# Performance work log

Measured on AMD Instinct MI355X. Metric: run time of the kernel, lower is better.

## Reference

```python
import jax, jax.numpy as jnp
import numpy as np

B, S, D, E, K = 4, 2048, 1024, 8, 2
DF = 4 * D


def setup_inputs() -> dict:
    key = jax.random.key(0)
    ks = jax.random.split(key, 7)
    x = jax.random.normal(ks[0], (B, S, D), dtype=jnp.float32)
    Wr = jax.random.normal(ks[1], (D, E), dtype=jnp.float32) * 0.02
    br = jnp.zeros((E,), dtype=jnp.float32)
    W1 = jax.random.normal(ks[2], (E, D, DF), dtype=jnp.float32) * 0.02
    b1 = jnp.zeros((E, DF), dtype=jnp.float32)
    W2 = jax.random.normal(ks[3], (E, DF, D), dtype=jnp.float32) * 0.02
    b2 = jnp.zeros((E, D), dtype=jnp.float32)
    return {"x": x, "Wr": Wr, "br": br, "W1": W1, "b1": b1, "W2": W2, "b2": b2}


def reference(x, Wr, br, W1, b1, W2, b2):
    # Router: softmax gates then top-k
    gates = jax.nn.softmax(x @ Wr + br, axis=-1)               # [B,S,E]
    topk_vals, topk_idx = jax.lax.top_k(gates, K)              # [B,S,K]

    # Per-(token, expert) combine weight: gate value if expert selected else 0
    onehot = jax.nn.one_hot(topk_idx, E, dtype=gates.dtype)    # [B,S,K,E]
    combine = jnp.sum(onehot * topk_vals[..., None], axis=2)   # [B,S,E]

    # Expert MLPs (loop over fixed small expert count, fully vectorized per expert)
    output = jnp.zeros_like(x)
    for e in range(E):
        h = jax.nn.gelu(x @ W1[e] + b1[e], approximate=False)  # [B,S,4D]
        y = h @ W2[e] + b2[e]                                  # [B,S,D]
        output = output + combine[..., e:e + 1] * y

    # Load-balancing aux loss (dispatch mask: 1.0 where expert selected)
    dispatch = jnp.max(onehot, axis=2)                         # [B,S,E]
    mean_gates = gates.mean(axis=(0, 1))
    mean_dispatch = dispatch.mean(axis=(0, 1))
    aux_loss = jnp.sum(mean_gates * mean_dispatch) * E / (B * S)
    return output, aux_loss
```

## Files before the change

### kernel.cpp

```cpp
#include <hip/hip_runtime.h>
#include <hip/hip_bf16.h>
#include <hip/hip_fp16.h>

typedef _Float16 f16;
typedef _Float16 half8 __attribute__((ext_vector_type(8)));
typedef _Float16 half4 __attribute__((ext_vector_type(4)));
typedef float   floatx4 __attribute__((ext_vector_type(4)));

#define N_TOK   8192
#define D_DIM   1024
#define E_NUM   8
#define DF_DIM  4096
#define MAX_SLOTS 18432
#define MAX_RT    72

#define MI_COUNT  0
#define MI_CURSOR 8
#define MI_OFF    16
#define MI_TOTAL  25
#define MI_RTE    26
#define MI_SUMG   168

__device__ __forceinline__ void gld_lds16(const void* g, void* l) {
    __builtin_amdgcn_global_load_lds(
        (__attribute__((address_space(1))) const void*)g,
        (__attribute__((address_space(3))) void*)l, 16, 0, 0);
}

__device__ __forceinline__ float gelu_f(float v) {
    float u = 0.7978845608028654f * v * (1.0f + 0.044715f * v * v);
    float t = __expf(-2.0f * fabsf(u));
    float th = (1.0f - t) / (1.0f + t);
    th = (u >= 0.f) ? th : -th;
    return 0.5f * v * (1.0f + th);
}

__global__ __launch_bounds__(256) void convert_x_kernel(
    const float* __restrict__ x, f16* __restrict__ xh)
{
    int idx = blockIdx.x * 256 + threadIdx.x;
    const int stride = gridDim.x * 256;
    const int n4 = (N_TOK * D_DIM) / 4;
    for (int i = idx; i < n4; i += stride) {
        float4 v = ((const float4*)x)[i];
        half4 o = { (f16)v.x, (f16)v.y, (f16)v.z, (f16)v.w };
        ((half4*)xh)[i] = o;
    }
}

__global__ __launch_bounds__(256) void transpose_conv_kernel(
    const float* __restrict__ src, f16* __restrict__ dst, int R, int C)
{
    const float* s = src + (size_t)blockIdx.z * R * C;
    f16* d = dst + (size_t)blockIdx.z * R * C;
    __shared__ float tile[64 * 65];
    const int rb = blockIdx.y * 64, cb = blockIdx.x * 64;
    const int tid = threadIdx.x;
#pragma unroll
    for (int j = 0; j < 4; ++j) {
        int lin = j * 1024 + tid * 4;
        int r = lin >> 6, c = lin & 63;
        float4 v = *(const float4*)(s + (size_t)(rb + r) * C + (cb + c));
        tile[r * 65 + c + 0] = v.x; tile[r * 65 + c + 1] = v.y;
        tile[r * 65 + c + 2] = v.z; tile[r * 65 + c + 3] = v.w;
    }
    __syncthreads();
#pragma unroll
    for (int j = 0; j < 4; ++j) {
        int lin = j * 1024 + tid * 4;
        int c = lin >> 6, r = lin & 63;
        half4 o = { (f16)tile[(r + 0) * 65 + c], (f16)tile[(r + 1) * 65 + c],
                    (f16)tile[(r + 2) * 65 + c], (f16)tile[(r + 3) * 65 + c] };
        *(half4*)(d + (size_t)(cb + c) * R + (rb + r)) = o;
    }
}

__global__ __launch_bounds__(256) void router_kernel(
    const float* __restrict__ x, const float* __restrict__ Wr,
    const float* __restrict__ br,
    int* __restrict__ topk_idx, float* __restrict__ topk_w,
    int* __restrict__ meta)
{
    const int w = threadIdx.x >> 6, l = threadIdx.x & 63;
    __shared__ float blk_sg[E_NUM];
    __shared__ int   blk_cnt[E_NUM];
    if (threadIdx.x < E_NUM) { blk_sg[threadIdx.x] = 0.f; blk_cnt[threadIdx.x] = 0; }
    __syncthreads();

    for (int it = 0; it < 4; ++it) {
        const int t = blockIdx.x * 16 + w * 4 + it;
        const float* xr = x + (size_t)t * D_DIM + l * 16;
        float acc[E_NUM] = {0.f,0.f,0.f,0.f,0.f,0.f,0.f,0.f};
#pragma unroll
        for (int i = 0; i < 16; i += 4) {
            float4 xv = *(const float4*)(xr + i);
            const float xs[4] = {xv.x, xv.y, xv.z, xv.w};
#pragma unroll
            for (int jj = 0; jj < 4; ++jj) {
                int d = l * 16 + i + jj;
                float4 w0 = *(const float4*)(Wr + (size_t)d * 8);
                float4 w1 = *(const float4*)(Wr + (size_t)d * 8 + 4);
                acc[0] += xs[jj] * w0.x; acc[1] += xs[jj] * w0.y;
                acc[2] += xs[jj] * w0.z; acc[3] += xs[jj] * w0.w;
                acc[4] += xs[jj] * w1.x; acc[5] += xs[jj] * w1.y;
                acc[6] += xs[jj] * w1.z; acc[7] += xs[jj] * w1.w;
            }
        }
#pragma unroll
        for (int e = 0; e < E_NUM; ++e) {
#pragma unroll
            for (int off = 32; off > 0; off >>= 1)
                acc[e] += __shfl_down(acc[e], off);
        }
        if (l == 0) {
            float lg[E_NUM], g[E_NUM];
            float mx = -1e30f;
#pragma unroll
            for (int e = 0; e < E_NUM; ++e) { lg[e] = acc[e] + br[e]; mx = fmaxf(mx, lg[e]); }
            float sum = 0.f;
#pragma unroll
            for (int e = 0; e < E_NUM; ++e) { g[e] = __expf(lg[e] - mx); sum += g[e]; }
            float inv = 1.f / sum;
#pragma unroll
            for (int e = 0; e < E_NUM; ++e) g[e] *= inv;
            int e1 = 0; float v1 = g[0];
#pragma unroll
            for (int e = 1; e < E_NUM; ++e) if (g[e] > v1) { v1 = g[e]; e1 = e; }
            int e2 = -1; float v2 = -1.f;
#pragma unroll
            for (int e = 0; e < E_NUM; ++e) if (e != e1 && g[e] > v2) { v2 = g[e]; e2 = e; }
            topk_idx[t * 2 + 0] = e1; topk_idx[t * 2 + 1] = e2;
            topk_w[t * 2 + 0] = v1;   topk_w[t * 2 + 1] = v2;
#pragma unroll
            for (int e = 0; e < E_NUM; ++e) atomicAdd(&blk_sg[e], g[e]);
            atomicAdd(&blk_cnt[e1], 1); atomicAdd(&blk_cnt[e2], 1);
        }
    }
    __syncthreads();
    if (threadIdx.x < E_NUM) {
        atomicAdd((float*)(meta + MI_SUMG) + threadIdx.x, blk_sg[threadIdx.x]);
        atomicAdd(meta + MI_COUNT + threadIdx.x, blk_cnt[threadIdx.x]);
    }
}

__global__ void scan_kernel(int* __restrict__ meta, float* __restrict__ out_aux)
{
    if (threadIdx.x != 0 || blockIdx.x != 0) return;
    int off = 0;
    for (int e = 0; e < E_NUM; ++e) {
        meta[MI_OFF + e] = off;
        int cnt = meta[MI_COUNT + e];
        int padded = ((cnt + 255) >> 8) << 8;
        for (int rt = off >> 8; rt < (off + padded) >> 8; ++rt)
            meta[MI_RTE + rt] = e;
        off += padded;
    }
    meta[MI_OFF + E_NUM] = off;
    meta[MI_TOTAL] = off >> 8;
    const float* sg = (const float*)(meta + MI_SUMG);
    float aux = 0.f;
    for (int e = 0; e < E_NUM; ++e)
        aux += (sg[e] / (float)N_TOK) * ((float)meta[MI_COUNT + e] / (float)N_TOK);
    out_aux[0] = aux * (float)E_NUM / (float)N_TOK;
}

__global__ __launch_bounds__(256) void fill_kernel(
    const int* __restrict__ topk_idx, const float* __restrict__ topk_w,
    int* __restrict__ meta, int* __restrict__ slot_token, float* __restrict__ slot_weight,
    int* __restrict__ slot_of)
{
    int t = blockIdx.x * 256 + threadIdx.x;
#pragma unroll
    for (int k = 0; k < 2; ++k) {
        int e = topk_idx[t * 2 + k];
        int p = atomicAdd(meta + MI_CURSOR + e, 1);
        int slot = meta[MI_OFF + e] + p;
        slot_token[slot] = t;
        slot_weight[slot] = topk_w[t * 2 + k];
        slot_of[t * 2 + k] = slot;
    }
}


#define STAGE_HALF(T, H) do {                                                  \
    f16* ld_ = smem + ((T)&1)*32768 + ((H)&1)*16384 + ((H)>>1)*8192;           \
    const f16* s0_ = ((H)&1) ? bsrc[((H)>>1)*2]     : asrc[((H)>>1)*2];        \
    const f16* s1_ = ((H)&1) ? bsrc[((H)>>1)*2 + 1] : asrc[((H)>>1)*2 + 1];    \
    gld_lds16(s0_ + (size_t)(T)*64, ld_ + tid*8);                              \
    gld_lds16(s1_ + (size_t)(T)*64, ld_ + 4096 + tid*8);                       \
} while(0)

#define READ_A(MH) do {                                                        \
    _Pragma("unroll")                                                          \
    for (int mj = 0; mj < 4; ++mj) {                                           \
        const f16* pa_ = LA + (size_t)(rA + (MH)*64 + mj*16) * 64;             \
        af[MH][mj][0] = *(const half8*)(pa_ + sw0);                            \
        af[MH][mj][1] = *(const half8*)(pa_ + sw1);                            \
    }                                                                          \
} while(0)

#define READ_B(NH) do {                                                        \
    _Pragma("unroll")                                                          \
    for (int nj = 0; nj < 2; ++nj) {                                           \
        const f16* pb_ = LB + (size_t)(rB + (NH)*32 + nj*16) * 64;             \
        bf[NH][nj][0] = *(const half8*)(pb_ + sw0);                            \
        bf[NH][nj][1] = *(const half8*)(pb_ + sw1);                            \
    }                                                                          \
} while(0)

#define MFMA_Q(MH, NH) do {                                                    \
    __builtin_amdgcn_s_setprio(1);                                             \
    _Pragma("unroll")                                                          \
    for (int mj = 0; mj < 4; ++mj)                                             \
    { _Pragma("unroll")                                                        \
      for (int nj = 0; nj < 2; ++nj) {                                         \
        acc[(MH)*4+mj][(NH)*2+nj] = __builtin_amdgcn_mfma_f32_16x16x32_f16(    \
            af[MH][mj][0], bf[NH][nj][0], acc[(MH)*4+mj][(NH)*2+nj], 0, 0, 0); \
        acc[(MH)*4+mj][(NH)*2+nj] = __builtin_amdgcn_mfma_f32_16x16x32_f16(    \
            af[MH][mj][1], bf[NH][nj][1], acc[(MH)*4+mj][(NH)*2+nj], 0, 0, 0); \
      } }                                                                      \
    __builtin_amdgcn_s_setprio(0);                                             \
} while(0)

template<int KD, int NCOLS, int KSPLIT, bool GATHER, bool GELU, bool BIAS>
__global__ __launch_bounds__(512, 2) void gemm256_kernel(
    const f16* __restrict__ A, const f16* __restrict__ Bw,
    const float* __restrict__ bias, const int* __restrict__ slot_token,
    const int* __restrict__ meta, f16* __restrict__ Out, size_t out_kp_stride)
{
    constexpr int KLOC = KD / KSPLIT;
    constexpr int NT = KLOC / 64;
    __shared__ __align__(16) f16 smem[65536];

    const int rt = blockIdx.y;
    if (rt >= meta[MI_TOTAL]) return;
    const int e  = meta[MI_RTE + rt];
    const int nt = blockIdx.x;
    const int kp = blockIdx.z;
    const int kbase = kp * KLOC;

    const int tid = threadIdx.x;
    const int w = tid >> 6, l = tid & 63;
    const int wr2 = w >> 2, wc2 = w & 3;
    const int fr = l & 15, fq = l >> 4;

    const int srow = tid >> 3;
    const int kcs  = (tid & 7) ^ (srow & 7);

    const f16* asrc[4]; const f16* bsrc[4];
#pragma unroll
    for (int i = 0; i < 4; ++i) {
        int r = ((i >> 1) * 128) + ((i & 1) * 64) + srow;
        int ar;
        if (GATHER) ar = slot_token[rt * 256 + r];
        else        ar = rt * 256 + r;
        asrc[i] = A + (size_t)ar * KD + kbase + kcs * 8;
        bsrc[i] = Bw + ((size_t)e * NCOLS + (size_t)nt * 256 + r) * KD + kbase + kcs * 8;
    }

    const int rA  = wr2 * 128 + fr;
    const int rB  = wc2 * 64 + fr;
    const int sw0 = ( fq      ^ (fr & 7)) * 8;
    const int sw1 = ((4 + fq) ^ (fr & 7)) * 8;

    floatx4 acc[8][4];
#pragma unroll
    for (int m = 0; m < 8; ++m)
#pragma unroll
        for (int n = 0; n < 4; ++n) acc[m][n] = (floatx4){0.f, 0.f, 0.f, 0.f};

    half8 af[2][4][2];
    half8 bf[2][2][2];

    STAGE_HALF(0, 0); STAGE_HALF(0, 1); STAGE_HALF(0, 2); STAGE_HALF(0, 3);
    if (NT > 1) STAGE_HALF(1, 0);
    asm volatile("s_waitcnt vmcnt(2)" ::: "memory");
    __builtin_amdgcn_s_barrier();

#pragma unroll 2
    for (int t = 0; t < NT; ++t) {
        const f16* LA = smem + (t & 1) * 32768;
        const f16* LB = LA + 16384;
        if (t + 1 < NT) { STAGE_HALF(t + 1, 1); STAGE_HALF(t + 1, 2); STAGE_HALF(t + 1, 3); }
        READ_A(0); READ_B(0); READ_B(1); READ_A(1);
        MFMA_Q(0, 0);
        MFMA_Q(0, 1);
        MFMA_Q(1, 0);
        if (t + 2 < NT) {
            asm volatile("s_waitcnt lgkmcnt(0)" ::: "memory");
            __builtin_amdgcn_s_barrier();
            STAGE_HALF(t + 2, 0);
        }
        MFMA_Q(1, 1);
        if (t + 1 < NT) {
            if (t + 1 < NT - 1) asm volatile("s_waitcnt vmcnt(2)" ::: "memory");
            else                asm volatile("s_waitcnt vmcnt(0)" ::: "memory");
            __builtin_amdgcn_s_barrier();
        }
    }

    f16* Op = Out + (size_t)kp * out_kp_stride;
    const int orow0 = rt * 256 + wr2 * 128;
    const int ocol0 = nt * 256 + wc2 * 64;
#pragma unroll
    for (int mi = 0; mi < 8; ++mi) {
#pragma unroll
        for (int n = 0; n < 4; ++n) {
            const int col = ocol0 + n * 16 + fr;
            float bs = 0.f;
            if (BIAS) bs = bias[(size_t)e * NCOLS + col];
#pragma unroll
            for (int j = 0; j < 4; ++j) {
                const int row = orow0 + mi * 16 + fq * 4 + j;
                float v = acc[mi][n][j] + bs;
                if (GELU) v = gelu_f(v);
                Op[(size_t)row * NCOLS + col] = (f16)v;
            }
        }
    }
}

__global__ __launch_bounds__(256) void combine_kernel(
    const f16* __restrict__ P, const int* __restrict__ slot_of,
    const int* __restrict__ topk_idx, const float* __restrict__ topk_w,
    const float* __restrict__ b2, float* __restrict__ out)
{
    const int t = blockIdx.x;
    const int c = threadIdx.x;
    const size_t PS = (size_t)MAX_SLOTS * D_DIM;
    const int s0 = slot_of[t * 2], s1 = slot_of[t * 2 + 1];
    const int e0 = topk_idx[t * 2], e1 = topk_idx[t * 2 + 1];
    const float w0 = topk_w[t * 2], w1 = topk_w[t * 2 + 1];
    half4 a0 = *(const half4*)(P + (size_t)s0 * D_DIM + c * 4);
    half4 a1 = *(const half4*)(P + PS + (size_t)s0 * D_DIM + c * 4);
    half4 c0 = *(const half4*)(P + (size_t)s1 * D_DIM + c * 4);
    half4 c1 = *(const half4*)(P + PS + (size_t)s1 * D_DIM + c * 4);
    float4 bb0 = *(const float4*)(b2 + (size_t)e0 * D_DIM + c * 4);
    float4 bb1 = *(const float4*)(b2 + (size_t)e1 * D_DIM + c * 4);
    float4 o;
    o.x = w0 * ((float)a0[0] + (float)a1[0] + bb0.x) + w1 * ((float)c0[0] + (float)c1[0] + bb1.x);
    o.y = w0 * ((float)a0[1] + (float)a1[1] + bb0.y) + w1 * ((float)c0[1] + (float)c1[1] + bb1.y);
    o.z = w0 * ((float)a0[2] + (float)a1[2] + bb0.z) + w1 * ((float)c0[2] + (float)c1[2] + bb1.z);
    o.w = w0 * ((float)a0[3] + (float)a1[3] + bb0.w) + w1 * ((float)c0[3] + (float)c1[3] + bb1.w);
    *(float4*)(out + (size_t)t * D_DIM + c * 4) = o;
}

extern "C" void kernel_launch(void* const* d_in, const int* in_sizes, int n_in,
                              void* d_out, int out_size, void* d_ws, size_t ws_size,
                              hipStream_t stream) {
    const float* x  = (const float*)d_in[0];
    const float* Wr = (const float*)d_in[1];
    const float* br = (const float*)d_in[2];
    const float* W1 = (const float*)d_in[3];
    const float* b1 = (const float*)d_in[4];
    const float* W2 = (const float*)d_in[5];
    const float* b2 = (const float*)d_in[6];
    float* out = (float*)d_out;

    char* ws = (char*)d_ws;
    const size_t SZ_XH  = (size_t)N_TOK * D_DIM * 2;
    const size_t SZ_W1T = (size_t)E_NUM * DF_DIM * D_DIM * 2;
    const size_t SZ_W2T = SZ_W1T;
    const size_t SZ_H   = (size_t)MAX_SLOTS * DF_DIM * 2;

    f16* xh  = (f16*)(ws);
    f16* W1t = (f16*)(ws + SZ_XH);
    f16* W2t = (f16*)(ws + SZ_XH + SZ_W1T);
    f16* H   = (f16*)(ws + SZ_XH + SZ_W1T + SZ_W2T);
    f16* P   = (f16*)ws;
    char* p  = ws + SZ_XH + SZ_W1T + SZ_W2T + SZ_H;
    int*   topk_idx    = (int*)p;    p += (size_t)N_TOK * 2 * 4;
    float* topk_w      = (float*)p;  p += (size_t)N_TOK * 2 * 4;
    int*   slot_token  = (int*)p;    p += (size_t)MAX_SLOTS * 4;
    float* slot_weight = (float*)p;  p += (size_t)MAX_SLOTS * 4;
    int*   slot_of     = (int*)p;    p += (size_t)N_TOK * 2 * 4;
    int*   meta        = (int*)p;

    hipMemsetAsync(slot_token, 0, (size_t)MAX_SLOTS * 8 + (size_t)N_TOK * 2 * 4 + 1024, stream);

    convert_x_kernel<<<2048, 256, 0, stream>>>(x, xh);
    transpose_conv_kernel<<<dim3(DF_DIM / 64, D_DIM / 64, E_NUM), 256, 0, stream>>>(W1, W1t, D_DIM, DF_DIM);
    transpose_conv_kernel<<<dim3(D_DIM / 64, DF_DIM / 64, E_NUM), 256, 0, stream>>>(W2, W2t, DF_DIM, D_DIM);
    router_kernel<<<N_TOK / 16, 256, 0, stream>>>(x, Wr, br, topk_idx, topk_w, meta);
    scan_kernel<<<1, 64, 0, stream>>>(meta, out + (size_t)N_TOK * D_DIM);
    fill_kernel<<<N_TOK / 256, 256, 0, stream>>>(topk_idx, topk_w, meta, slot_token, slot_weight, slot_of);

    gemm256_kernel<D_DIM, DF_DIM, 1, true, true, true>
        <<<dim3(DF_DIM / 256, MAX_RT, 1), 512, 0, stream>>>(
        xh, W1t, b1, slot_token, meta, H, 0);

    gemm256_kernel<DF_DIM, D_DIM, 2, false, false, false>
        <<<dim3(D_DIM / 256, MAX_RT, 2), 512, 0, stream>>>(
        H, W2t, nullptr, slot_token, meta, P, (size_t)MAX_SLOTS * D_DIM);

    combine_kernel<<<N_TOK, 256, 0, stream>>>(P, slot_of, topk_idx, topk_w, b2, out);

    (void)in_sizes; (void)n_in; (void)ws_size;
}
```

Baseline: 617.8 us.

## Shrink grouped GEMM tiles from 256x256 to 128x128 with finer expert padding

Rewrites the grouped expert GEMM to use 128x128 output tiles with half the LDS, fewer accumulators, and an occupancy hint of 4 blocks per CU. Per-expert row padding drops from 256 to 128 slots, so less padding work is wasted and there are more tiles to spread across CUs. The staging and barrier pipeline is restructured to match. In exchange, each loaded byte is reused less (lower arithmetic intensity), there are more block launches, and there are more barriers per unit of compute.

```diff
diff --git a/kernel.cpp b/kernel.cpp
--- a/kernel.cpp
+++ b/kernel.cpp
@@ -11,8 +11,8 @@
 #define D_DIM   1024
 #define E_NUM   8
 #define DF_DIM  4096
-#define MAX_SLOTS 18432
-#define MAX_RT    72
+#define MAX_SLOTS 17408
+#define MAX_RT    136
 
 #define MI_COUNT  0
 #define MI_CURSOR 8
@@ -150,13 +150,13 @@
     for (int e = 0; e < E_NUM; ++e) {
         meta[MI_OFF + e] = off;
         int cnt = meta[MI_COUNT + e];
-        int padded = ((cnt + 255) >> 8) << 8;
-        for (int rt = off >> 8; rt < (off + padded) >> 8; ++rt)
+        int padded = ((cnt + 127) >> 7) << 7;
+        for (int rt = off >> 7; rt < (off + padded) >> 7; ++rt)
             meta[MI_RTE + rt] = e;
         off += padded;
     }
     meta[MI_OFF + E_NUM] = off;
-    meta[MI_TOTAL] = off >> 8;
+    meta[MI_TOTAL] = off >> 7;
     const float* sg = (const float*)(meta + MI_SUMG);
     float aux = 0.f;
     for (int e = 0; e < E_NUM; ++e)
@@ -183,54 +183,47 @@
 
 
 #define STAGE_HALF(T, H) do {                                                  \
-    f16* ld_ = smem + ((T)&1)*32768 + ((H)&1)*16384 + ((H)>>1)*8192;           \
-    const f16* s0_ = ((H)&1) ? bsrc[((H)>>1)*2]     : asrc[((H)>>1)*2];        \
-    const f16* s1_ = ((H)&1) ? bsrc[((H)>>1)*2 + 1] : asrc[((H)>>1)*2 + 1];    \
-    gld_lds16(s0_ + (size_t)(T)*64, ld_ + tid*8);                              \
-    gld_lds16(s1_ + (size_t)(T)*64, ld_ + 4096 + tid*8);                       \
+    f16* ld_ = smem + ((T)&1)*16384 + ((H)&1)*8192 + ((H)>>1)*4096;            \
+    const f16* s_ = ((H)&1) ? bsrc[(H)>>1] : asrc[(H)>>1];                     \
+    gld_lds16(s_ + (size_t)(T)*64, ld_ + tid*8);                               \
 } while(0)
 
-#define READ_A(MH) do {                                                        \
+#define READ_AB() do {                                                         \
     _Pragma("unroll")                                                          \
     for (int mj = 0; mj < 4; ++mj) {                                           \
-        const f16* pa_ = LA + (size_t)(rA + (MH)*64 + mj*16) * 64;             \
-        af[MH][mj][0] = *(const half8*)(pa_ + sw0);                            \
-        af[MH][mj][1] = *(const half8*)(pa_ + sw1);                            \
+        const f16* pa_ = LA + (size_t)(rA + mj*16) * 64;                       \
+        af[mj][0] = *(const half8*)(pa_ + sw0);                                \
+        af[mj][1] = *(const half8*)(pa_ + sw1);                                \
+    }                                                                          \
+    _Pragma("unroll")                                                          \
+    for (int nj = 0; nj < 2; ++nj) {                                           \
+        const f16* pb_ = LB + (size_t)(rB + nj*16) * 64;                       \
+        bf[nj][0] = *(const half8*)(pb_ + sw0);                                \
+        bf[nj][1] = *(const half8*)(pb_ + sw1);                                \
     }                                                                          \
 } while(0)
 
-#define READ_B(NH) do {                                                        \
+#define MFMA_MJ(MJ) do {                                                       \
+    __builtin_amdgcn_s_setprio(1);                                             \
     _Pragma("unroll")                                                          \
     for (int nj = 0; nj < 2; ++nj) {                                           \
-        const f16* pb_ = LB + (size_t)(rB + (NH)*32 + nj*16) * 64;             \
-        bf[NH][nj][0] = *(const half8*)(pb_ + sw0);                            \
-        bf[NH][nj][1] = *(const half8*)(pb_ + sw1);                            \
+        acc[MJ][nj] = __builtin_amdgcn_mfma_f32_16x16x32_f16(                  \
+            af[MJ][0], bf[nj][0], acc[MJ][nj], 0, 0, 0);                       \
+        acc[MJ][nj] = __builtin_amdgcn_mfma_f32_16x16x32_f16(                  \
+            af[MJ][1], bf[nj][1], acc[MJ][nj], 0, 0, 0);                       \
     }                                                                          \
-} while(0)
-
-#define MFMA_Q(MH, NH) do {                                                    \
-    __builtin_amdgcn_s_setprio(1);                                             \
-    _Pragma("unroll")                                                          \
-    for (int mj = 0; mj < 4; ++mj)                                             \
-    { _Pragma("unroll")                                                        \
-      for (int nj = 0; nj < 2; ++nj) {                                         \
-        acc[(MH)*4+mj][(NH)*2+nj] = __builtin_amdgcn_mfma_f32_16x16x32_f16(    \
-            af[MH][mj][0], bf[NH][nj][0], acc[(MH)*4+mj][(NH)*2+nj], 0, 0, 0); \
-        acc[(MH)*4+mj][(NH)*2+nj] = __builtin_amdgcn_mfma_f32_16x16x32_f16(    \
-            af[MH][mj][1], bf[NH][nj][1], acc[(MH)*4+mj][(NH)*2+nj], 0, 0, 0); \
-      } }                                                                      \
     __builtin_amdgcn_s_setprio(0);                                             \
 } while(0)
 
 template<int KD, int NCOLS, int KSPLIT, bool GATHER, bool GELU, bool BIAS>
-__global__ __launch_bounds__(512, 2) void gemm256_kernel(
+__global__ __launch_bounds__(512, 4) void gemm128_kernel(
     const f16* __restrict__ A, const f16* __restrict__ Bw,
     const float* __restrict__ bias, const int* __restrict__ slot_token,
     const int* __restrict__ meta, f16* __restrict__ Out, size_t out_kp_stride)
 {
     constexpr int KLOC = KD / KSPLIT;
     constexpr int NT = KLOC / 64;
-    __shared__ __align__(16) f16 smem[65536];
+    __shared__ __align__(16) f16 smem[32768];
 
     const int rt = blockIdx.y;
     if (rt >= meta[MI_TOTAL]) return;
@@ -247,72 +240,68 @@
     const int srow = tid >> 3;
     const int kcs  = (tid & 7) ^ (srow & 7);
 
-    const f16* asrc[4]; const f16* bsrc[4];
-#pragma unroll
-    for (int i = 0; i < 4; ++i) {
-        int r = ((i >> 1) * 128) + ((i & 1) * 64) + srow;
+    const f16* asrc[2]; const f16* bsrc[2];
+#pragma unroll
+    for (int i = 0; i < 2; ++i) {
+        int r = i * 64 + srow;
         int ar;
-        if (GATHER) ar = slot_token[rt * 256 + r];
-        else        ar = rt * 256 + r;
+        if (GATHER) ar = slot_token[rt * 128 + r];
+        else        ar = rt * 128 + r;
         asrc[i] = A + (size_t)ar * KD + kbase + kcs * 8;
-        bsrc[i] = Bw + ((size_t)e * NCOLS + (size_t)nt * 256 + r) * KD + kbase + kcs * 8;
-    }
-
-    const int rA  = wr2 * 128 + fr;
-    const int rB  = wc2 * 64 + fr;
+        bsrc[i] = Bw + ((size_t)e * NCOLS + (size_t)nt * 128 + r) * KD + kbase + kcs * 8;
+    }
+
+    const int rA  = wr2 * 64 + fr;
+    const int rB  = wc2 * 32 + fr;
     const int sw0 = ( fq      ^ (fr & 7)) * 8;
     const int sw1 = ((4 + fq) ^ (fr & 7)) * 8;
 
-    floatx4 acc[8][4];
-#pragma unroll
-    for (int m = 0; m < 8; ++m)
-#pragma unroll
-        for (int n = 0; n < 4; ++n) acc[m][n] = (floatx4){0.f, 0.f, 0.f, 0.f};
-
-    half8 af[2][4][2];
-    half8 bf[2][2][2];
+    floatx4 acc[4][2];
+#pragma unroll
+    for (int m = 0; m < 4; ++m)
+#pragma unroll
+        for (int n = 0; n < 2; ++n) acc[m][n] = (floatx4){0.f, 0.f, 0.f, 0.f};
+
+    half8 af[4][2];
+    half8 bf[2][2];
 
     STAGE_HALF(0, 0); STAGE_HALF(0, 1); STAGE_HALF(0, 2); STAGE_HALF(0, 3);
-    if (NT > 1) STAGE_HALF(1, 0);
-    asm volatile("s_waitcnt vmcnt(2)" ::: "memory");
+    STAGE_HALF(1, 0);
+    asm volatile("s_waitcnt vmcnt(1)" ::: "memory");
     __builtin_amdgcn_s_barrier();
 
 #pragma unroll 2
     for (int t = 0; t < NT; ++t) {
-        const f16* LA = smem + (t & 1) * 32768;
-        const f16* LB = LA + 16384;
+        const f16* LA = smem + (t & 1) * 16384;
+        const f16* LB = LA + 8192;
         if (t + 1 < NT) { STAGE_HALF(t + 1, 1); STAGE_HALF(t + 1, 2); STAGE_HALF(t + 1, 3); }
-        READ_A(0); READ_B(0); READ_B(1); READ_A(1);
-        MFMA_Q(0, 0);
-        MFMA_Q(0, 1);
-        MFMA_Q(1, 0);
-        if (t + 2 < NT) {
-            asm volatile("s_waitcnt lgkmcnt(0)" ::: "memory");
-            __builtin_amdgcn_s_barrier();
-            STAGE_HALF(t + 2, 0);
-        }
-        MFMA_Q(1, 1);
+        READ_AB();
+        MFMA_MJ(0); MFMA_MJ(1); MFMA_MJ(2);
+        asm volatile("s_waitcnt lgkmcnt(0)" ::: "memory");
+        __builtin_amdgcn_s_barrier();
+        if (t + 2 < NT) STAGE_HALF(t + 2, 0);
+        MFMA_MJ(3);
         if (t + 1 < NT) {
-            if (t + 1 < NT - 1) asm volatile("s_waitcnt vmcnt(2)" ::: "memory");
+            if (t + 1 < NT - 1) asm volatile("s_waitcnt vmcnt(1)" ::: "memory");
             else                asm volatile("s_waitcnt vmcnt(0)" ::: "memory");
             __builtin_amdgcn_s_barrier();
         }
     }
 
     f16* Op = Out + (size_t)kp * out_kp_stride;
-    const int orow0 = rt * 256 + wr2 * 128;
-    const int ocol0 = nt * 256 + wc2 * 64;
-#pragma unroll
-    for (int mi = 0; mi < 8; ++mi) {
-#pragma unroll
-        for (int n = 0; n < 4; ++n) {
-            const int col = ocol0 + n * 16 + fr;
+    const int orow0 = rt * 128 + wr2 * 64;
+    const int ocol0 = nt * 128 + wc2 * 32;
+#pragma unroll
+    for (int mj = 0; mj < 4; ++mj) {
+#pragma unroll
+        for (int nj = 0; nj < 2; ++nj) {
+            const int col = ocol0 + nj * 16 + fr;
             float bs = 0.f;
             if (BIAS) bs = bias[(size_t)e * NCOLS + col];
 #pragma unroll
             for (int j = 0; j < 4; ++j) {
-                const int row = orow0 + mi * 16 + fq * 4 + j;
-                float v = acc[mi][n][j] + bs;
+                const int row = orow0 + mj * 16 + fq * 4 + j;
+                float v = acc[mj][nj][j] + bs;
                 if (GELU) v = gelu_f(v);
                 Op[(size_t)row * NCOLS + col] = (f16)v;
             }
@@ -385,12 +374,12 @@
     scan_kernel<<<1, 64, 0, stream>>>(meta, out + (size_t)N_TOK * D_DIM);
     fill_kernel<<<N_TOK / 256, 256, 0, stream>>>(topk_idx, topk_w, meta, slot_token, slot_weight, slot_of);
 
-    gemm256_kernel<D_DIM, DF_DIM, 1, true, true, true>
-        <<<dim3(DF_DIM / 256, MAX_RT, 1), 512, 0, stream>>>(
+    gemm128_kernel<D_DIM, DF_DIM, 1, true, true, true>
+        <<<dim3(DF_DIM / 128, MAX_RT, 1), 512, 0, stream>>>(
         xh, W1t, b1, slot_token, meta, H, 0);
 
-    gemm256_kernel<DF_DIM, D_DIM, 2, false, false, false>
-        <<<dim3(D_DIM / 256, MAX_RT, 2), 512, 0, stream>>>(
+    gemm128_kernel<DF_DIM, D_DIM, 2, false, false, false>
+        <<<dim3(D_DIM / 128, MAX_RT, 2), 512, 0, stream>>>(
         H, W2t, nullptr, slot_token, meta, P, (size_t)MAX_SLOTS * D_DIM);
 
     combine_kernel<<<N_TOK, 256, 0, stream>>>(P, slot_of, topk_idx, topk_w, b2, out);
```

New measurement: 635.7 us. 1.03x slower.
